# Kernel tuning notes

Hardware: AMD Instinct MI355X
Metric: run time of the kernel (lower is better)

Reference implementation:

```python
import jax, jax.numpy as jnp
import numpy as np

EPS = 1e-5

def _layernorm(x, g, b):
    mu = jnp.mean(x, axis=-1, keepdims=True)
    var = jnp.mean(jnp.square(x - mu), axis=-1, keepdims=True)
    return (x - mu) * jax.lax.rsqrt(var + EPS) * g + b

def setup_inputs() -> dict:
    key = jax.random.key(0)
    ks = jax.random.split(key, 6)
    B, S, D = 4, 2048, 1024
    F = 4 * D
    return {
        "hidden_states": jax.random.normal(ks[0], (B, S, D), jnp.float32),
        "w_qkv": jax.random.normal(ks[1], (D, 3 * D), jnp.float32) * (D ** -0.5),
        "fc1_w": jax.random.normal(ks[2], (D, F), jnp.float32) * (D ** -0.5),
        "fc1_b": jax.random.normal(ks[3], (F,), jnp.float32) * 0.02,
        "fc2_w": jax.random.normal(ks[4], (F, D), jnp.float32) * (F ** -0.5),
        "fc2_b": jax.random.normal(ks[5], (D,), jnp.float32) * 0.02,
        "ln1_g": jnp.ones((D,), jnp.float32),
        "ln1_b": jnp.zeros((D,), jnp.float32),
        "ln2_g": jnp.ones((D,), jnp.float32),
        "ln2_b": jnp.zeros((D,), jnp.float32),
    }

def reference(hidden_states, w_qkv, fc1_w, fc1_b, fc2_w, fc2_b, ln1_g, ln1_b, ln2_g, ln2_b):
    D = hidden_states.shape[-1]
    residual = hidden_states
    h = _layernorm(hidden_states, ln1_g, ln1_b)
    qkv = jnp.einsum('bsd,de->bse', h, w_qkv)  # [B,S,3D]
    q, k, v = jnp.split(qkv, 3, axis=-1)
    # single-head attention, NO 1/sqrt(d) scaling, no mask (faithful to source)
    scores = jnp.einsum('bsd,btd->bst', q, k)  # [B,S,S]
    w = jax.nn.softmax(scores, axis=-1)
    attn = jnp.einsum('bst,btd->bsd', w, v)
    h = attn + residual
    residual = h
    h = _layernorm(h, ln2_g, ln2_b)
    h = jnp.einsum('bsd,df->bsf', h, fc1_w) + fc1_b
    h = jax.nn.gelu(h, approximate=False)  # torch nn.GELU default is exact erf
    h = jnp.einsum('bsf,fd->bsd', h, fc2_w) + fc2_b
    return h + residual
```

## Files before the change

kernel.cpp:

```cpp
#include <hip/hip_runtime.h>
#include <math.h>

typedef unsigned short u16;
typedef unsigned int u32;
typedef _Float16 f16x8 __attribute__((ext_vector_type(8)));
typedef float f32x4 __attribute__((ext_vector_type(4)));
typedef u16 u16x4 __attribute__((ext_vector_type(4)));

__device__ __forceinline__ u16 f2h(float x) {
  _Float16 h = (_Float16)x;
  return __builtin_bit_cast(u16, h);
}
__device__ __forceinline__ float h2f(u16 u) {
  return (float)__builtin_bit_cast(_Float16, u);
}

__device__ __forceinline__ float gelu_erf(float x) {
  const float u = x * 0.70710678118654752f;
  const float s = fabsf(u);
  const float t = __frcp_rn(1.0f + 0.3275911f * s);
  float p = 1.061405429f;
  p = p * t - 1.453152027f;
  p = p * t + 1.421413741f;
  p = p * t - 0.284496736f;
  p = p * t + 0.254829592f;
  const float e = __expf(-s * s);
  float erf = 1.0f - p * t * e;
  erf = u < 0.0f ? -erf : erf;
  return 0.5f * x * (1.0f + erf);
}

__device__ __forceinline__ void gload16(const void* g, void* l) {
  __builtin_amdgcn_global_load_lds(
      (const __attribute__((address_space(1))) void*)g,
      (__attribute__((address_space(3))) void*)l, 16, 0, 0);
}

template <int EPI, bool SWZ>
__global__ __launch_bounds__(256, 4) void gemm_nt(
    const u16* __restrict__ A, const u16* __restrict__ B, int M, int N, int K,
    int lda, int ldb, long zsA, long zsB, long zsC, float* __restrict__ outF,
    u16* __restrict__ outU, u16* __restrict__ outU2,
    const float* __restrict__ aux0, const float* __restrict__ aux1) {
  __shared__ char smem[2 * 128 * 64 * 2];
  char* sA = smem;
  char* sB = smem + 16384;

  const int tid = threadIdx.x;
  const int lane = tid & 63;
  const int wave = tid >> 6;
  const int z = blockIdx.z;

  int bx = blockIdx.x, by = blockIdx.y;
  if constexpr (SWZ) {
    const int gx = gridDim.x;
    const int nwg = gx * gridDim.y;
    const int id = by * gx + bx;
    const int q = nwg >> 3;
    const int id2 = (id & 7) * q + (id >> 3);
    bx = id2 % gx;
    by = id2 / gx;
  }
  const long row0 = (long)by * 128;
  const long col0 = (long)bx * 128;

  const u16* __restrict__ Ab = A + (long)z * zsA;
  const u16* __restrict__ Bb = B + (long)z * zsB;

  const int srow = lane >> 3;
  const int sslot = (lane & 7) ^ srow;

  const int wm = (wave >> 1) << 6;
  const int wn = (wave & 1) << 6;
  const int fr = lane & 15;
  const int kgrp = lane >> 4;

  f32x4 acc[4][4] = {};
  const int nk = K >> 6;

  auto stage = [&](int kt) {
#pragma unroll
    for (int c = 0; c < 4; ++c) {
      const int chunk = wave * 4 + c;
      const int r = chunk * 8 + srow;
      gload16(Ab + (row0 + r) * (long)lda + kt * 64 + sslot * 8,
              sA + chunk * 1024);
      gload16(Bb + (col0 + r) * (long)ldb + kt * 64 + sslot * 8,
              sB + chunk * 1024);
    }
  };

  stage(0);
  for (int kt = 0; kt < nk; ++kt) {
    __syncthreads();
#pragma unroll
    for (int kk = 0; kk < 2; ++kk) {
      f16x8 af[4], bg[4];
#pragma unroll
      for (int i = 0; i < 4; ++i) {
        const int r = wm + i * 16 + fr;
        const int slot = ((kk << 2) | kgrp) ^ (r & 7);
        af[i] = *(const f16x8*)(sA + r * 128 + slot * 16);
      }
#pragma unroll
      for (int j = 0; j < 4; ++j) {
        const int r = wn + j * 16 + fr;
        const int slot = ((kk << 2) | kgrp) ^ (r & 7);
        bg[j] = *(const f16x8*)(sB + r * 128 + slot * 16);
      }
#pragma unroll
      for (int i = 0; i < 4; ++i)
#pragma unroll
        for (int j = 0; j < 4; ++j)
          acc[i][j] = __builtin_amdgcn_mfma_f32_16x16x32_f16(af[i], bg[j],
                                                             acc[i][j], 0, 0, 0);
    }
    __syncthreads();
    if (kt + 1 < nk) stage(kt + 1);
  }

#pragma unroll
  for (int i = 0; i < 4; ++i) {
#pragma unroll
    for (int j = 0; j < 4; ++j) {
#pragma unroll
      for (int r = 0; r < 4; ++r) {
        const long m = row0 + wm + i * 16 + (kgrp << 2) + r;
        const long n = col0 + wn + j * 16 + fr;
        const float val = acc[i][j][r];
        if constexpr (EPI == 0) {
          if (n < 2048)
            outU[m * 2048 + n] = f2h(val);
          else
            outU2[m * 1024 + (n - 2048)] = f2h(val);
        } else if constexpr (EPI == 1) {
          outF[(long)z * zsC + m * (long)N + n] = val;
        } else if constexpr (EPI == 2) {
          const long idx = (long)z * zsC + m * (long)N + n;
          outF[idx] = val + aux0[idx];
        } else if constexpr (EPI == 3) {
          outU[m * (long)N + n] = f2h(gelu_erf(val + aux0[n]));
        } else {
          outF[m * (long)N + n] = val + aux0[n] + aux1[m * (long)N + n];
        }
      }
    }
  }
}

__global__ __launch_bounds__(256) void ln_k(const float* __restrict__ x,
                                            const float* __restrict__ gw,
                                            const float* __restrict__ bw,
                                            u16* __restrict__ out) {
  const int lane = threadIdx.x & 63;
  const int wv = threadIdx.x >> 6;
  const long row = (long)blockIdx.x * 4 + wv;
  const float* xr = x + row * 1024;
  float4 v[4];
  float s = 0.f, ss = 0.f;
#pragma unroll
  for (int j = 0; j < 4; ++j) {
    v[j] = *(const float4*)(xr + (lane + 64 * j) * 4);
    s += v[j].x + v[j].y + v[j].z + v[j].w;
    ss += v[j].x * v[j].x + v[j].y * v[j].y + v[j].z * v[j].z + v[j].w * v[j].w;
  }
#pragma unroll
  for (int o = 32; o; o >>= 1) {
    s += __shfl_xor(s, o);
    ss += __shfl_xor(ss, o);
  }
  const float mu = s * (1.f / 1024.f);
  const float var = ss * (1.f / 1024.f) - mu * mu;
  const float rs = rsqrtf(var + 1e-5f);
  u16* orow = out + row * 1024;
#pragma unroll
  for (int j = 0; j < 4; ++j) {
    const int n = (lane + 64 * j) * 4;
    const float4 gg = *(const float4*)(gw + n);
    const float4 bb = *(const float4*)(bw + n);
    u16x4 H;
    H[0] = f2h((v[j].x - mu) * rs * gg.x + bb.x);
    H[1] = f2h((v[j].y - mu) * rs * gg.y + bb.y);
    H[2] = f2h((v[j].z - mu) * rs * gg.z + bb.z);
    H[3] = f2h((v[j].w - mu) * rs * gg.w + bb.w);
    *(u16x4*)(orow + n) = H;
  }
}

template <int MODE>
__global__ __launch_bounds__(256) void transpose_k(const void* __restrict__ in,
                                                   u16* __restrict__ out,
                                                   int R, int C, long zsIn,
                                                   long zsOut) {
  __shared__ float tile[32][33];
  const int z = blockIdx.z;
  const int c0 = blockIdx.x * 32, r0 = blockIdx.y * 32;
#pragma unroll
  for (int i = 0; i < 4; ++i) {
    const int lin = threadIdx.x + 256 * i;
    const int rr = lin >> 5, cc = lin & 31;
    float vv;
    if constexpr (MODE == 2)
      vv = h2f(((const u16*)in + (long)z * zsIn)[(long)(r0 + rr) * C + c0 + cc]);
    else
      vv = ((const float*)in)[(long)(r0 + rr) * C + c0 + cc];
    tile[rr][cc] = vv;
  }
  __syncthreads();
  u16* outz = out + (long)z * zsOut;
#pragma unroll
  for (int i = 0; i < 4; ++i) {
    const int lin = threadIdx.x + 256 * i;
    const int oc = lin >> 5, orr = lin & 31;
    outz[(long)(c0 + oc) * R + (r0 + orr)] = f2h(tile[orr][oc]);
  }
}

__global__ __launch_bounds__(256) void softmax_k(float* __restrict__ S) {
  const long row = blockIdx.x;
  float* sr = S + row * 2048;
  u16* pr = (u16*)sr;
  const int tid = threadIdx.x;
  const int lane = tid & 63, wv = tid >> 6;
  __shared__ float red[8];
  const float4 v0 = *(const float4*)(sr + tid * 4);
  const float4 v1 = *(const float4*)(sr + 1024 + tid * 4);
  float mx = fmaxf(fmaxf(fmaxf(v0.x, v0.y), fmaxf(v0.z, v0.w)),
                   fmaxf(fmaxf(v1.x, v1.y), fmaxf(v1.z, v1.w)));
#pragma unroll
  for (int o = 32; o; o >>= 1) mx = fmaxf(mx, __shfl_xor(mx, o));
  if (lane == 0) red[wv] = mx;
  __syncthreads();
  mx = fmaxf(fmaxf(red[0], red[1]), fmaxf(red[2], red[3]));
  float e[8];
  e[0] = __expf(v0.x - mx); e[1] = __expf(v0.y - mx);
  e[2] = __expf(v0.z - mx); e[3] = __expf(v0.w - mx);
  e[4] = __expf(v1.x - mx); e[5] = __expf(v1.y - mx);
  e[6] = __expf(v1.z - mx); e[7] = __expf(v1.w - mx);
  float sm = e[0] + e[1] + e[2] + e[3] + e[4] + e[5] + e[6] + e[7];
#pragma unroll
  for (int o = 32; o; o >>= 1) sm += __shfl_xor(sm, o);
  if (lane == 0) red[4 + wv] = sm;
  __syncthreads();
  sm = red[4] + red[5] + red[6] + red[7];
  const float inv = 1.f / sm;
  u16x4 a, b;
  a[0] = f2h(e[0] * inv); a[1] = f2h(e[1] * inv);
  a[2] = f2h(e[2] * inv); a[3] = f2h(e[3] * inv);
  b[0] = f2h(e[4] * inv); b[1] = f2h(e[5] * inv);
  b[2] = f2h(e[6] * inv); b[3] = f2h(e[7] * inv);
  *(u16x4*)(pr + tid * 4) = a;
  *(u16x4*)(pr + 1024 + tid * 4) = b;
}

extern "C" void kernel_launch(void* const* d_in, const int* in_sizes, int n_in,
                              void* d_out, int out_size, void* d_ws,
                              size_t ws_size, hipStream_t stream) {
  const float* x     = (const float*)d_in[0];
  const float* w_qkv = (const float*)d_in[1];
  const float* fc1_w = (const float*)d_in[2];
  const float* fc1_b = (const float*)d_in[3];
  const float* fc2_w = (const float*)d_in[4];
  const float* fc2_b = (const float*)d_in[5];
  const float* ln1_g = (const float*)d_in[6];
  const float* ln1_b = (const float*)d_in[7];
  const float* ln2_g = (const float*)d_in[8];
  const float* ln2_b = (const float*)d_in[9];
  float* out = (float*)d_out;

  char* ws = (char*)d_ws;
  const long MB = 1024L * 1024L;
  u16*   h    = (u16*)(ws + 0);
  u16*   wqkT = (u16*)(ws + 16 * MB);
  float* sc   = (float*)(ws + 0);
  u16*   qk   = (u16*)(ws + 64 * MB);
  u16*   vbuf = (u16*)(ws + 96 * MB);
  u16*   vT   = (u16*)(ws + 112 * MB);
  u16*   w1T  = (u16*)(ws + 144 * MB);
  u16*   w2T  = (u16*)(ws + 152 * MB);
  float* r2   = (float*)(ws + 64 * MB);
  u16*   h2   = (u16*)(ws + 96 * MB);
  u16*   g    = (u16*)(ws + 0);

  dim3 blk(256);

  ln_k<<<2048, blk, 0, stream>>>(x, ln1_g, ln1_b, h);
  transpose_k<0><<<dim3(3072 / 32, 1024 / 32, 1), blk, 0, stream>>>(
      w_qkv, wqkT, 1024, 3072, 0, 0);
  gemm_nt<0, true><<<dim3(24, 64, 1), blk, 0, stream>>>(
      h, wqkT, 8192, 3072, 1024, 1024, 1024, 0, 0, 0, nullptr, qk, vbuf,
      nullptr, nullptr);
  transpose_k<2><<<dim3(1024 / 32, 2048 / 32, 4), blk, 0, stream>>>(
      vbuf, vT, 2048, 1024, 2048L * 1024, 1024L * 2048);
  gemm_nt<1, true><<<dim3(16, 16, 4), blk, 0, stream>>>(
      qk, qk + 1024, 2048, 2048, 1024, 2048, 2048, 2048L * 2048, 2048L * 2048,
      2048L * 2048, sc, nullptr, nullptr, nullptr, nullptr);
  softmax_k<<<8192, blk, 0, stream>>>(sc);
  gemm_nt<2, true><<<dim3(8, 16, 4), blk, 0, stream>>>(
      (const u16*)sc, vT, 2048, 1024, 2048, 4096, 2048, 2048L * 4096,
      1024L * 2048, 2048L * 1024, r2, nullptr, nullptr, x, nullptr);
  ln_k<<<2048, blk, 0, stream>>>(r2, ln2_g, ln2_b, h2);
  transpose_k<0><<<dim3(4096 / 32, 1024 / 32, 1), blk, 0, stream>>>(
      fc1_w, w1T, 1024, 4096, 0, 0);
  transpose_k<0><<<dim3(1024 / 32, 4096 / 32, 1), blk, 0, stream>>>(
      fc2_w, w2T, 4096, 1024, 0, 0);
  gemm_nt<3, true><<<dim3(32, 64, 1), blk, 0, stream>>>(
      h2, w1T, 8192, 4096, 1024, 1024, 1024, 0, 0, 0, nullptr, g, nullptr,
      fc1_b, nullptr);
  gemm_nt<4, true><<<dim3(8, 64, 1), blk, 0, stream>>>(
      g, w2T, 8192, 1024, 4096, 4096, 4096, 0, 0, 0, out, nullptr, nullptr,
      fc2_b, r2);
}
```

Baseline: 375.1 us.

## Switch GEMM to 32x32 MFMA, fuse V transpose into QKV epilogue, fp16 residual

Replaces the 16x16x32 MFMA tiling with 32x32x16 instructions using 2x2 accumulators per wave, which cuts LDS fragment loads per MFMA. The QKV GEMM epilogue now writes V directly in transposed layout, removing the separate V transpose kernel. The attention+residual output is stored as fp16 and read by the second layernorm and the final epilogue as fp16, halving that traffic at the cost of residual precision.

Result: slower. 401.9 us (+7.1%).

```diff
diff --git a/kernel.cpp b/kernel.cpp
--- a/kernel.cpp
+++ b/kernel.cpp
@@ -4,7 +4,7 @@
 typedef unsigned short u16;
 typedef unsigned int u32;
 typedef _Float16 f16x8 __attribute__((ext_vector_type(8)));
-typedef float f32x4 __attribute__((ext_vector_type(4)));
+typedef float f32x16 __attribute__((ext_vector_type(16)));
 typedef u16 u16x4 __attribute__((ext_vector_type(4)));
 
 __device__ __forceinline__ u16 f2h(float x) {
@@ -41,7 +41,7 @@
     const u16* __restrict__ A, const u16* __restrict__ B, int M, int N, int K,
     int lda, int ldb, long zsA, long zsB, long zsC, float* __restrict__ outF,
     u16* __restrict__ outU, u16* __restrict__ outU2,
-    const float* __restrict__ aux0, const float* __restrict__ aux1) {
+    const float* __restrict__ aux0, const u16* __restrict__ aux1u) {
   __shared__ char smem[2 * 128 * 64 * 2];
   char* sA = smem;
   char* sB = smem + 16384;
@@ -70,12 +70,12 @@
   const int srow = lane >> 3;
   const int sslot = (lane & 7) ^ srow;
 
+  const int ln31 = lane & 31;
+  const int hh = lane >> 5;
   const int wm = (wave >> 1) << 6;
   const int wn = (wave & 1) << 6;
-  const int fr = lane & 15;
-  const int kgrp = lane >> 4;
-
-  f32x4 acc[4][4] = {};
+
+  f32x16 acc[2][2] = {};
   const int nk = K >> 6;
 
   auto stage = [&](int kt) {
@@ -94,25 +94,25 @@
   for (int kt = 0; kt < nk; ++kt) {
     __syncthreads();
 #pragma unroll
-    for (int kk = 0; kk < 2; ++kk) {
-      f16x8 af[4], bg[4];
-#pragma unroll
-      for (int i = 0; i < 4; ++i) {
-        const int r = wm + i * 16 + fr;
-        const int slot = ((kk << 2) | kgrp) ^ (r & 7);
+    for (int ks = 0; ks < 4; ++ks) {
+      f16x8 af[2], bg[2];
+#pragma unroll
+      for (int i = 0; i < 2; ++i) {
+        const int r = wm + i * 32 + ln31;
+        const int slot = ((ks << 1) | hh) ^ (r & 7);
         af[i] = *(const f16x8*)(sA + r * 128 + slot * 16);
       }
 #pragma unroll
-      for (int j = 0; j < 4; ++j) {
-        const int r = wn + j * 16 + fr;
-        const int slot = ((kk << 2) | kgrp) ^ (r & 7);
+      for (int j = 0; j < 2; ++j) {
+        const int r = wn + j * 32 + ln31;
+        const int slot = ((ks << 1) | hh) ^ (r & 7);
         bg[j] = *(const f16x8*)(sB + r * 128 + slot * 16);
       }
 #pragma unroll
-      for (int i = 0; i < 4; ++i)
-#pragma unroll
-        for (int j = 0; j < 4; ++j)
-          acc[i][j] = __builtin_amdgcn_mfma_f32_16x16x32_f16(af[i], bg[j],
+      for (int i = 0; i < 2; ++i)
+#pragma unroll
+        for (int j = 0; j < 2; ++j)
+          acc[i][j] = __builtin_amdgcn_mfma_f32_32x32x16_f16(af[i], bg[j],
                                                              acc[i][j], 0, 0, 0);
     }
     __syncthreads();
@@ -120,47 +120,72 @@
   }
 
 #pragma unroll
-  for (int i = 0; i < 4; ++i) {
-#pragma unroll
-    for (int j = 0; j < 4; ++j) {
-#pragma unroll
-      for (int r = 0; r < 4; ++r) {
-        const long m = row0 + wm + i * 16 + (kgrp << 2) + r;
-        const long n = col0 + wn + j * 16 + fr;
-        const float val = acc[i][j][r];
+  for (int i = 0; i < 2; ++i) {
+#pragma unroll
+    for (int j = 0; j < 2; ++j) {
+      const long n = col0 + wn + j * 32 + ln31;
+#pragma unroll
+      for (int q = 0; q < 4; ++q) {
+        const long mb = row0 + wm + i * 32 + (q << 3) + (hh << 2);
         if constexpr (EPI == 0) {
-          if (n < 2048)
-            outU[m * 2048 + n] = f2h(val);
-          else
-            outU2[m * 1024 + (n - 2048)] = f2h(val);
+          if (n < 2048) {
+#pragma unroll
+            for (int rr = 0; rr < 4; ++rr)
+              outU[(mb + rr) * 2048 + n] = f2h(acc[i][j][4 * q + rr]);
+          } else {
+            u16x4 V;
+#pragma unroll
+            for (int rr = 0; rr < 4; ++rr) V[rr] = f2h(acc[i][j][4 * q + rr]);
+            *(u16x4*)(outU2 + ((mb >> 11) << 21) + (n - 2048) * 2048 +
+                      (mb & 2047)) = V;
+          }
         } else if constexpr (EPI == 1) {
-          outF[(long)z * zsC + m * (long)N + n] = val;
+#pragma unroll
+          for (int rr = 0; rr < 4; ++rr)
+            outF[(long)z * zsC + (mb + rr) * (long)N + n] = acc[i][j][4 * q + rr];
         } else if constexpr (EPI == 2) {
-          const long idx = (long)z * zsC + m * (long)N + n;
-          outF[idx] = val + aux0[idx];
+#pragma unroll
+          for (int rr = 0; rr < 4; ++rr) {
+            const long idx = (long)z * zsC + (mb + rr) * (long)N + n;
+            outU[idx] = f2h(acc[i][j][4 * q + rr] + aux0[idx]);
+          }
         } else if constexpr (EPI == 3) {
-          outU[m * (long)N + n] = f2h(gelu_erf(val + aux0[n]));
+          const float b = aux0[n];
+#pragma unroll
+          for (int rr = 0; rr < 4; ++rr)
+            outU[(mb + rr) * (long)N + n] = f2h(gelu_erf(acc[i][j][4 * q + rr] + b));
         } else {
-          outF[m * (long)N + n] = val + aux0[n] + aux1[m * (long)N + n];
+          const float b = aux0[n];
+#pragma unroll
+          for (int rr = 0; rr < 4; ++rr) {
+            const long idx = (mb + rr) * (long)N + n;
+            outF[idx] = acc[i][j][4 * q + rr] + b + h2f(aux1u[idx]);
+          }
         }
       }
     }
   }
 }
 
-__global__ __launch_bounds__(256) void ln_k(const float* __restrict__ x,
+template <bool F32IN>
+__global__ __launch_bounds__(256) void ln_k(const void* __restrict__ xin,
                                             const float* __restrict__ gw,
                                             const float* __restrict__ bw,
                                             u16* __restrict__ out) {
   const int lane = threadIdx.x & 63;
   const int wv = threadIdx.x >> 6;
   const long row = (long)blockIdx.x * 4 + wv;
-  const float* xr = x + row * 1024;
   float4 v[4];
   float s = 0.f, ss = 0.f;
 #pragma unroll
   for (int j = 0; j < 4; ++j) {
-    v[j] = *(const float4*)(xr + (lane + 64 * j) * 4);
+    const int n = (lane + 64 * j) * 4;
+    if constexpr (F32IN) {
+      v[j] = *(const float4*)((const float*)xin + row * 1024 + n);
+    } else {
+      const u16x4 hv = *(const u16x4*)((const u16*)xin + row * 1024 + n);
+      v[j] = make_float4(h2f(hv[0]), h2f(hv[1]), h2f(hv[2]), h2f(hv[3]));
+    }
     s += v[j].x + v[j].y + v[j].z + v[j].w;
     ss += v[j].x * v[j].x + v[j].y * v[j].y + v[j].z * v[j].z + v[j].w * v[j].w;
   }
@@ -187,32 +212,23 @@
   }
 }
 
-template <int MODE>
-__global__ __launch_bounds__(256) void transpose_k(const void* __restrict__ in,
+__global__ __launch_bounds__(256) void transpose_k(const float* __restrict__ in,
                                                    u16* __restrict__ out,
-                                                   int R, int C, long zsIn,
-                                                   long zsOut) {
+                                                   int R, int C) {
   __shared__ float tile[32][33];
-  const int z = blockIdx.z;
   const int c0 = blockIdx.x * 32, r0 = blockIdx.y * 32;
 #pragma unroll
   for (int i = 0; i < 4; ++i) {
     const int lin = threadIdx.x + 256 * i;
     const int rr = lin >> 5, cc = lin & 31;
-    float vv;
-    if constexpr (MODE == 2)
-      vv = h2f(((const u16*)in + (long)z * zsIn)[(long)(r0 + rr) * C + c0 + cc]);
-    else
-      vv = ((const float*)in)[(long)(r0 + rr) * C + c0 + cc];
-    tile[rr][cc] = vv;
+    tile[rr][cc] = in[(long)(r0 + rr) * C + c0 + cc];
   }
   __syncthreads();
-  u16* outz = out + (long)z * zsOut;
 #pragma unroll
   for (int i = 0; i < 4; ++i) {
     const int lin = threadIdx.x + 256 * i;
     const int oc = lin >> 5, orr = lin & 31;
-    outz[(long)(c0 + oc) * R + (r0 + orr)] = f2h(tile[orr][oc]);
+    out[(long)(c0 + oc) * R + (r0 + orr)] = f2h(tile[orr][oc]);
   }
 }
 
@@ -274,36 +290,33 @@
   u16*   wqkT = (u16*)(ws + 16 * MB);
   float* sc   = (float*)(ws + 0);
   u16*   qk   = (u16*)(ws + 64 * MB);
-  u16*   vbuf = (u16*)(ws + 96 * MB);
+  u16*   h2   = (u16*)(ws + 96 * MB);
   u16*   vT   = (u16*)(ws + 112 * MB);
   u16*   w1T  = (u16*)(ws + 144 * MB);
   u16*   w2T  = (u16*)(ws + 152 * MB);
-  float* r2   = (float*)(ws + 64 * MB);
-  u16*   h2   = (u16*)(ws + 96 * MB);
+  u16*   r2   = (u16*)(ws + 160 * MB);
   u16*   g    = (u16*)(ws + 0);
 
   dim3 blk(256);
 
-  ln_k<<<2048, blk, 0, stream>>>(x, ln1_g, ln1_b, h);
-  transpose_k<0><<<dim3(3072 / 32, 1024 / 32, 1), blk, 0, stream>>>(
-      w_qkv, wqkT, 1024, 3072, 0, 0);
+  ln_k<true><<<2048, blk, 0, stream>>>(x, ln1_g, ln1_b, h);
+  transpose_k<<<dim3(3072 / 32, 1024 / 32, 1), blk, 0, stream>>>(w_qkv, wqkT,
+                                                                 1024, 3072);
   gemm_nt<0, true><<<dim3(24, 64, 1), blk, 0, stream>>>(
-      h, wqkT, 8192, 3072, 1024, 1024, 1024, 0, 0, 0, nullptr, qk, vbuf,
+      h, wqkT, 8192, 3072, 1024, 1024, 1024, 0, 0, 0, nullptr, qk, vT,
       nullptr, nullptr);
-  transpose_k<2><<<dim3(1024 / 32, 2048 / 32, 4), blk, 0, stream>>>(
-      vbuf, vT, 2048, 1024, 2048L * 1024, 1024L * 2048);
   gemm_nt<1, true><<<dim3(16, 16, 4), blk, 0, stream>>>(
       qk, qk + 1024, 2048, 2048, 1024, 2048, 2048, 2048L * 2048, 2048L * 2048,
       2048L * 2048, sc, nullptr, nullptr, nullptr, nullptr);
   softmax_k<<<8192, blk, 0, stream>>>(sc);
   gemm_nt<2, true><<<dim3(8, 16, 4), blk, 0, stream>>>(
       (const u16*)sc, vT, 2048, 1024, 2048, 4096, 2048, 2048L * 4096,
-      1024L * 2048, 2048L * 1024, r2, nullptr, nullptr, x, nullptr);
-  ln_k<<<2048, blk, 0, stream>>>(r2, ln2_g, ln2_b, h2);
-  transpose_k<0><<<dim3(4096 / 32, 1024 / 32, 1), blk, 0, stream>>>(
-      fc1_w, w1T, 1024, 4096, 0, 0);
-  transpose_k<0><<<dim3(1024 / 32, 4096 / 32, 1), blk, 0, stream>>>(
-      fc2_w, w2T, 4096, 1024, 0, 0);
+      1024L * 2048, 2048L * 1024, nullptr, r2, nullptr, x, nullptr);
+  ln_k<false><<<2048, blk, 0, stream>>>(r2, ln2_g, ln2_b, h2);
+  transpose_k<<<dim3(4096 / 32, 1024 / 32, 1), blk, 0, stream>>>(fc1_w, w1T,
+                                                                 1024, 4096);
+  transpose_k<<<dim3(1024 / 32, 4096 / 32, 1), blk, 0, stream>>>(fc2_w, w2T,
+                                                                 4096, 1024);
   gemm_nt<3, true><<<dim3(32, 64, 1), blk, 0, stream>>>(
       h2, w1T, 8192, 4096, 1024, 1024, 1024, 0, 0, 0, nullptr, g, nullptr,
       fc1_b, nullptr);
```
